# Optimization experiments

Measured on AMD Instinct MI355X. Metric: run time of the kernel, lower is better.

The kernel has to match this reference:

```python
import math
import jax, jax.numpy as jnp
import numpy as np

# TreeAttention (HiP-style hierarchical top-k mask) hyperparameters
K = 64          # self.k: retained keys per query
W0 = 64         # self.w: initial coarse window
SCALE_UP = 2.0
OVERSAMPLE = 1.5
NEG = -32000.0  # masked score fill used inside the pruning loop
FMIN = -1e30    # masked score fill for final softmax


def _gather_rows(m, idx):
    # m: [N, C, H], idx: [N, A, Z] -> [N, A, Z, H]
    return jnp.take_along_axis(m[:, None, :, :], idx[:, :, :, None], axis=2)


def _masked_scores(q, k, xs, xs_mask, value):
    # jax equivalent of masked_bmm_masked_indices (sampled_addmm on a CSR mask):
    # only compute q . k[xs] at the Z listed columns per query row.
    C = k.shape[1]
    kg = _gather_rows(k, jnp.minimum(xs, C - 1))          # [N, A, Z, H]
    s = jnp.einsum('nah,nazh->naz', q, kg)
    return jnp.where(xs_mask > 0.5, s, value)


def _dedup_rows(ps):
    # ps: [R, L] sorted ascending per row. Replicates torch
    # unique_consecutive(return_inverse) + per-row min-subtract + scatter:
    # compact distinct values to the front, fill the rest with -1.
    first = jnp.ones((ps.shape[0], 1), dtype=bool)
    is_new = jnp.concatenate([first, ps[:, 1:] != ps[:, :-1]], axis=1)
    ranks = jnp.cumsum(is_new, axis=1) - 1                # rank of distinct value in row
    rows = jnp.arange(ps.shape[0])[:, None]
    out = jnp.full_like(ps, -1)
    return out.at[rows, ranks].set(ps)  # duplicate ranks write identical values


def _forward_mask(q, k):
    N, T_SRC, HID = k.shape
    _, T_DST, _ = q.shape
    start = T_SRC - T_DST + 1
    tsrcs = jnp.arange(start, start + T_DST, dtype=jnp.float32)[None, :, None]  # [1,T_DST,1]
    w = W0
    ws = jnp.full((N, T_DST, 1), float(W0), dtype=jnp.float32)
    max_pixels = max(int(round(K * OVERSAMPLE)), W0)
    pixels = jnp.broadcast_to(jnp.arange(max_pixels, dtype=jnp.int32)[None, None, :],
                              (N, T_DST, max_pixels))
    pmask = jnp.broadcast_to((jnp.arange(max_pixels) < W0).astype(jnp.float32)[None, None, :],
                             (N, T_DST, max_pixels))
    MAX_SU = int(math.ceil(SCALE_UP))
    while True:  # static loop: w doubles 64 -> 4096, 7 iterations
        is_last = (w == T_SRC)
        Z = pixels.shape[-1]
        # --- topk_mask: score the current candidate pixels, keep top tks ---
        txs = jnp.round(pixels * (tsrcs / ws)).astype(jnp.int32)
        scores = _masked_scores(q, k, txs, pmask, NEG)
        mult = 1.0 if is_last else OVERSAMPLE
        tks = jnp.clip(jnp.round(ws / tsrcs * K * mult), 1.0,
                       jnp.minimum(ws - 1.0, float(Z - 1))).astype(jnp.int32)  # [N,T_DST,1]
        tks_max = int(math.ceil(min(w - 1, Z - 1, K * mult)))
        _, idx = jax.lax.top_k(scores, tks_max)
        new_pixels = jnp.take_along_axis(pixels, idx, axis=-1)
        new_pmask = (jnp.arange(tks_max)[None, None, :] < tks).astype(jnp.float32)
        pixels = jnp.pad(new_pixels, ((0, 0), (0, 0), (0, Z - tks_max)))
        pmask = jnp.pad(new_pmask, ((0, 0), (0, 0), (0, Z - tks_max)))
        # --- update per-row window, then resize pixels into the finer grid ---
        ws_new = jnp.minimum(tsrcs, ws * SCALE_UP)
        scale = ws_new / ws
        ps_start = jnp.round(pixels * scale).astype(jnp.int32)
        ps_end = jnp.round((pixels + 1) * scale).astype(jnp.int32)
        ps = jnp.broadcast_to(ps_start[..., None], (N, T_DST, Z, MAX_SU))
        counts = (ps_end - ps_start)[..., None]
        reps = jnp.arange(MAX_SU, dtype=jnp.float32)[None, None, None, :] * pmask[..., None]
        ps = ps + jnp.minimum(reps, jnp.maximum(counts - 1, 0).astype(jnp.float32)).astype(jnp.int32)
        ps = jnp.sort(ps.reshape(N * T_DST, Z * MAX_SU), axis=-1)
        ps = _dedup_rows(ps).reshape(N, T_DST, -1)
        pmask = (ps >= 0).astype(jnp.float32)
        pixels = jnp.where(ps < 0, 0, ps)
        max_z = K if is_last else int(round(K * 2))
        pixels = pixels[..., :max_z]
        pmask = pmask[..., :max_z]
        ws = ws_new
        if is_last:
            break
        w = min(T_SRC, w * SCALE_UP)
    return pixels, pmask  # CSR mask: per-query column indices + validity mask


def setup_inputs() -> dict:
    key = jax.random.key(0)
    kq, kk, kv = jax.random.split(key, 3)
    N, T_DST, T_SRC, HID = 8, 512, 4096, 64
    q = jax.random.normal(kq, (N, T_DST, HID), dtype=jnp.float32)
    k = jax.random.normal(kk, (N, T_SRC, HID), dtype=jnp.float32)
    v = jax.random.normal(kv, (N, T_SRC, HID), dtype=jnp.float32)
    return {"q": q, "k": k, "v": v}


def reference(q, k, v):
    pixels, pmask = _forward_mask(q, k)          # [N,T_DST,K] int, [N,T_DST,K] {0,1}
    kg = _gather_rows(k, pixels)                 # [N,T_DST,K,H]
    vg = _gather_rows(v, pixels)
    s = jnp.einsum('nah,nazh->naz', q, kg)
    s = jnp.where(pmask > 0.5, s, FMIN)
    p = jax.nn.softmax(s, axis=-1)
    return jnp.einsum('naz,nazh->nah', p, vg)    # [N, T_DST, HID]
```

## Files before the change

kernel.cpp:

```cpp
#include <hip/hip_runtime.h>
#include <math.h>


#define TSRC_N 4096
#define HID_N  64
#define NEGV   -32000.0f

__global__ __launch_bounds__(256)
void tree_attn_kernel(const float* __restrict__ q,
                      const float* __restrict__ k,
                      const float* __restrict__ v,
                      float* __restrict__ out)
{
    const int wid  = __builtin_amdgcn_readfirstlane((int)(threadIdx.x >> 6));
    const int lane = threadIdx.x & 63;
    const int row  = (blockIdx.x << 2) + wid;
    const int n    = row >> 9;
    const float tsrc = (float)(3585 + (row & 511));

    __shared__ __align__(16) unsigned int key_s[4][128];
    __shared__ __align__(16) unsigned int bm[4][128];
    __shared__ int                        pix_s[4][128];
    __shared__ unsigned char              msk_s[4][128];
    __shared__ __align__(8) unsigned int  pp_s[4][128];
    unsigned int* const keyw = key_s[wid];
    unsigned int* const bmw  = bm[wid];
    int* const           pixw = pix_s[wid];
    unsigned char* const mskw = msk_s[wid];
    unsigned int* const  ppw  = pp_s[wid];

    const float* qrow = q + (size_t)row * HID_N;
    const float* kb   = k + (size_t)n * TSRC_N * HID_N;
    const float* vb   = v + (size_t)n * TSRC_N * HID_N;

    auto dot_f32 = [&](int tx) -> float {
        const float4* k4 = (const float4*)(kb + (size_t)tx * HID_N);
        float a0 = 0.f, a1 = 0.f, a2 = 0.f, a3 = 0.f;
        #pragma unroll
        for (int h4 = 0; h4 < HID_N / 4; ++h4) {
            const float4 kv = k4[h4];
            a0 = fmaf(kv.x, qrow[h4 * 4 + 0], a0);
            a1 = fmaf(kv.y, qrow[h4 * 4 + 1], a1);
            a2 = fmaf(kv.z, qrow[h4 * 4 + 2], a2);
            a3 = fmaf(kv.w, qrow[h4 * 4 + 3], a3);
        }
        return (a0 + a1) + (a2 + a3);
    };
    auto flip32 = [](float s) -> unsigned int {
        const unsigned int u = __float_as_uint(s);
        return u ^ ((unsigned)((int)u >> 31) | 0x80000000u);
    };

    pixw[lane]      = lane;
    pixw[lane + 64] = lane + 64;
    mskw[lane]      = 1;
    mskw[lane + 64] = 0;
    __builtin_amdgcn_wave_barrier();

    float ws = 64.0f;
    int Z = 96;

    for (int it = 0; it < 7; ++it) {
        const bool  last    = (it == 6);
        const float mult    = last ? 1.0f : 1.5f;
        const int   tks_max = (it == 0) ? 63 : (last ? 64 : 96);
        const int   max_z   = last ? 64 : 128;
        const int   e1      = lane + 64;

        const float r = tsrc / ws;
        unsigned int key0 = 0, key1 = 0;
        {
            float s0 = NEGV;
            if (mskw[lane]) {
                int tx = (int)rintf((float)pixw[lane] * r);
                tx = tx < (TSRC_N - 1) ? tx : (TSRC_N - 1);
                s0 = dot_f32(tx);
            }
            key0 = flip32(s0);
        }
        if (e1 < Z) {
            float s1 = NEGV;
            if (mskw[e1]) {
                int tx = (int)rintf((float)pixw[e1] * r);
                tx = tx < (TSRC_N - 1) ? tx : (TSRC_N - 1);
                s1 = dot_f32(tx);
            }
            key1 = flip32(s1);
        }
        keyw[lane] = key0;
        keyw[e1]   = key1;
        bmw[lane]  = 0u;
        bmw[e1]    = 0u;
        __builtin_amdgcn_wave_barrier();

        int r0 = 0, r1 = 0;
        #pragma unroll 8
        for (int j = 0; j < 128; j += 4) {
            const uint4 kk = *(const uint4*)&keyw[j];
            r0 += (int)(kk.x > key0) + (int)(kk.y > key0)
                + (int)(kk.z > key0) + (int)(kk.w > key0);
            r1 += (int)(kk.x > key1) + (int)(kk.y > key1)
                + (int)(kk.z > key1) + (int)(kk.w > key1);
        }

        float x = ws / tsrc;
        x *= 64.0f;
        x *= mult;
        float t = rintf(x);
        t = fmaxf(1.0f, fminf(t, fminf(ws - 1.0f, (float)(Z - 1))));
        const int tks = (int)t;

        const float ws_new = fminf(tsrc, ws * 2.0f);
        const float scale  = ws_new / ws;

        if (lane == 0) atomicOr(&bmw[0], 1u);
        if (r0 < tks_max) {
            const int p  = pixw[lane];
            int s0 = (int)rintf((float)p * scale);
            s0 = s0 < (TSRC_N - 1) ? s0 : (TSRC_N - 1);
            atomicOr(&bmw[s0 >> 5], 1u << (s0 & 31));
            if (r0 < tks) {
                const int s1i = (int)rintf((float)(p + 1) * scale);
                if (s1i - s0 >= 2) {
                    const int c = s0 + 1;
                    atomicOr(&bmw[c >> 5], 1u << (c & 31));
                }
            }
        }
        if (e1 < Z && r1 < tks_max) {
            const int p  = pixw[e1];
            int s0 = (int)rintf((float)p * scale);
            s0 = s0 < (TSRC_N - 1) ? s0 : (TSRC_N - 1);
            atomicOr(&bmw[s0 >> 5], 1u << (s0 & 31));
            if (r1 < tks) {
                const int s1i = (int)rintf((float)(p + 1) * scale);
                if (s1i - s0 >= 2) {
                    const int c = s0 + 1;
                    atomicOr(&bmw[c >> 5], 1u << (c & 31));
                }
            }
        }
        __builtin_amdgcn_wave_barrier();

        const uint2 w2 = *(const uint2*)&bmw[2 * lane];
        const int c = __popc(w2.x) + __popc(w2.y);
        int scan = c;
        #pragma unroll
        for (int off = 1; off < 64; off <<= 1) {
            const int o = __shfl_up(scan, off);
            if (lane >= off) scan += o;
        }
        int pref = scan - c;
        pixw[lane] = 0;  pixw[e1] = 0;
        mskw[lane] = 0;  mskw[e1] = 0;
        __builtin_amdgcn_wave_barrier();

        unsigned int wv = w2.x;
        int base = lane << 6;
        while (wv) {
            if (pref >= max_z) break;
            const int b = __ffs(wv) - 1;
            wv &= wv - 1u;
            pixw[pref] = base + b;
            mskw[pref] = 1;
            ++pref;
        }
        wv = w2.y;
        base += 32;
        while (wv) {
            if (pref >= max_z) break;
            const int b = __ffs(wv) - 1;
            wv &= wv - 1u;
            pixw[pref] = base + b;
            mskw[pref] = 1;
            ++pref;
        }
        __builtin_amdgcn_wave_barrier();

        ws = ws_new;
        Z  = max_z;
    }

    {
        const int pix = pixw[lane];
        float sfin = -1e30f;
        if (mskw[lane]) sfin = dot_f32(pix);
        float m = sfin;
        #pragma unroll
        for (int off = 32; off > 0; off >>= 1)
            m = fmaxf(m, __shfl_xor(m, off));
        const float e = __expf(sfin - m);
        float ssum = e;
        #pragma unroll
        for (int off = 32; off > 0; off >>= 1)
            ssum += __shfl_xor(ssum, off);
        const float p = e / ssum;
        ppw[2 * lane]     = __float_as_uint(p);
        ppw[2 * lane + 1] = (unsigned int)pix;
    }
    __builtin_amdgcn_wave_barrier();

    {
        float acc = 0.f;
        #pragma unroll 4
        for (int j = 0; j < 64; ++j) {
            const uint2 pp = *(const uint2*)&ppw[2 * j];
            acc = fmaf(__uint_as_float(pp.x),
                       vb[(size_t)pp.y * HID_N + lane], acc);
        }
        out[(size_t)row * HID_N + lane] = acc;
    }
}

extern "C" void kernel_launch(void* const* d_in, const int* in_sizes, int n_in,
                              void* d_out, int out_size, void* d_ws, size_t ws_size,
                              hipStream_t stream) {
    const float* q = (const float*)d_in[0];
    const float* k = (const float*)d_in[1];
    const float* v = (const float*)d_in[2];
    float* out = (float*)d_out;
    const int rows = in_sizes[0] / HID_N;
    tree_attn_kernel<<<(rows + 3) / 4, 256, 0, stream>>>(q, k, v, out);
}
```

Baseline: 163.9 us.

## Split each query row across two wavefronts with block-level sync

Each query row is now handled by a pair of wavefronts instead of one, so each lane scores one candidate instead of two. The final PV accumulation is split across the pair and combined through shared memory. The dot product is software-pipelined with explicit prefetch, and launch bounds now request higher occupancy. The cost is wave-level barriers replaced by block-wide __syncthreads, twice as many blocks, and the redundant prefix scan and compaction now run in both waves of a pair.

```diff
diff --git a/kernel.cpp b/kernel.cpp
--- a/kernel.cpp
+++ b/kernel.cpp
@@ -6,28 +6,34 @@
 #define HID_N  64
 #define NEGV   -32000.0f
 
-__global__ __launch_bounds__(256)
+__global__ __launch_bounds__(256, 8)
 void tree_attn_kernel(const float* __restrict__ q,
                       const float* __restrict__ k,
                       const float* __restrict__ v,
                       float* __restrict__ out)
 {
-    const int wid  = __builtin_amdgcn_readfirstlane((int)(threadIdx.x >> 6));
+    const int wid4 = __builtin_amdgcn_readfirstlane((int)(threadIdx.x >> 6));
     const int lane = threadIdx.x & 63;
-    const int row  = (blockIdx.x << 2) + wid;
+    const int pairid = wid4 >> 1;
+    const int sub    = wid4 & 1;
+    const int row  = (blockIdx.x << 1) + pairid;
     const int n    = row >> 9;
     const float tsrc = (float)(3585 + (row & 511));
-
-    __shared__ __align__(16) unsigned int key_s[4][128];
-    __shared__ __align__(16) unsigned int bm[4][128];
-    __shared__ int                        pix_s[4][128];
-    __shared__ unsigned char              msk_s[4][128];
-    __shared__ __align__(8) unsigned int  pp_s[4][128];
-    unsigned int* const keyw = key_s[wid];
-    unsigned int* const bmw  = bm[wid];
-    int* const           pixw = pix_s[wid];
-    unsigned char* const mskw = msk_s[wid];
-    unsigned int* const  ppw  = pp_s[wid];
+    const int e    = (sub << 6) + lane;
+
+    __shared__ __align__(16) unsigned int key_s[2][128];
+    __shared__ __align__(16) unsigned int bm_s[2][128];
+    __shared__ int                        pix_s[2][128];
+    __shared__ unsigned char              msk_s[2][128];
+    __shared__ __align__(8) unsigned int  pp_s[2][128];
+    __shared__ float                      part_s[2][64];
+
+    unsigned int*  const keyw  = key_s[pairid];
+    unsigned int*  const bmw   = bm_s[pairid];
+    int*           const pixw  = pix_s[pairid];
+    unsigned char* const mskw  = msk_s[pairid];
+    unsigned int*  const ppw   = pp_s[pairid];
+    float*         const partw = part_s[pairid];
 
     const float* qrow = q + (size_t)row * HID_N;
     const float* kb   = k + (size_t)n * TSRC_N * HID_N;
@@ -35,14 +41,24 @@
 
     auto dot_f32 = [&](int tx) -> float {
         const float4* k4 = (const float4*)(kb + (size_t)tx * HID_N);
+        float4 c0 = k4[0], c1 = k4[1], c2 = k4[2], c3 = k4[3];
         float a0 = 0.f, a1 = 0.f, a2 = 0.f, a3 = 0.f;
         #pragma unroll
-        for (int h4 = 0; h4 < HID_N / 4; ++h4) {
-            const float4 kv = k4[h4];
-            a0 = fmaf(kv.x, qrow[h4 * 4 + 0], a0);
-            a1 = fmaf(kv.y, qrow[h4 * 4 + 1], a1);
-            a2 = fmaf(kv.z, qrow[h4 * 4 + 2], a2);
-            a3 = fmaf(kv.w, qrow[h4 * 4 + 3], a3);
+        for (int g = 0; g < 4; ++g) {
+            float4 n0, n1, n2, n3;
+            if (g < 3) {
+                n0 = k4[4*g+4]; n1 = k4[4*g+5]; n2 = k4[4*g+6]; n3 = k4[4*g+7];
+            }
+            const float* qg = qrow + 16*g;
+            a0 = fmaf(c0.x, qg[0],  a0);  a1 = fmaf(c0.y, qg[1],  a1);
+            a2 = fmaf(c0.z, qg[2],  a2);  a3 = fmaf(c0.w, qg[3],  a3);
+            a0 = fmaf(c1.x, qg[4],  a0);  a1 = fmaf(c1.y, qg[5],  a1);
+            a2 = fmaf(c1.z, qg[6],  a2);  a3 = fmaf(c1.w, qg[7],  a3);
+            a0 = fmaf(c2.x, qg[8],  a0);  a1 = fmaf(c2.y, qg[9],  a1);
+            a2 = fmaf(c2.z, qg[10], a2);  a3 = fmaf(c2.w, qg[11], a3);
+            a0 = fmaf(c3.x, qg[12], a0);  a1 = fmaf(c3.y, qg[13], a1);
+            a2 = fmaf(c3.z, qg[14], a2);  a3 = fmaf(c3.w, qg[15], a3);
+            if (g < 3) { c0 = n0; c1 = n1; c2 = n2; c3 = n3; }
         }
         return (a0 + a1) + (a2 + a3);
     };
@@ -51,11 +67,9 @@
         return u ^ ((unsigned)((int)u >> 31) | 0x80000000u);
     };
 
-    pixw[lane]      = lane;
-    pixw[lane + 64] = lane + 64;
-    mskw[lane]      = 1;
-    mskw[lane + 64] = 0;
-    __builtin_amdgcn_wave_barrier();
+    pixw[e] = e;
+    mskw[e] = (e < 64) ? 1 : 0;
+    __syncthreads();
 
     float ws = 64.0f;
     int Z = 96;
@@ -65,42 +79,39 @@
         const float mult    = last ? 1.0f : 1.5f;
         const int   tks_max = (it == 0) ? 63 : (last ? 64 : 96);
         const int   max_z   = last ? 64 : 128;
-        const int   e1      = lane + 64;
 
         const float r = tsrc / ws;
-        unsigned int key0 = 0, key1 = 0;
-        {
-            float s0 = NEGV;
-            if (mskw[lane]) {
-                int tx = (int)rintf((float)pixw[lane] * r);
+        unsigned int mykey = 0;
+        int myp = 0;
+        if (e < Z) {
+            float sc = NEGV;
+            myp = pixw[e];
+            if (mskw[e]) {
+                int tx = (int)rintf((float)myp * r);
                 tx = tx < (TSRC_N - 1) ? tx : (TSRC_N - 1);
-                s0 = dot_f32(tx);
+                sc = dot_f32(tx);
             }
-            key0 = flip32(s0);
-        }
-        if (e1 < Z) {
-            float s1 = NEGV;
-            if (mskw[e1]) {
-                int tx = (int)rintf((float)pixw[e1] * r);
-                tx = tx < (TSRC_N - 1) ? tx : (TSRC_N - 1);
-                s1 = dot_f32(tx);
-            }
-            key1 = flip32(s1);
-        }
-        keyw[lane] = key0;
-        keyw[e1]   = key1;
-        bmw[lane]  = 0u;
-        bmw[e1]    = 0u;
-        __builtin_amdgcn_wave_barrier();
-
-        int r0 = 0, r1 = 0;
-        #pragma unroll 8
-        for (int j = 0; j < 128; j += 4) {
-            const uint4 kk = *(const uint4*)&keyw[j];
-            r0 += (int)(kk.x > key0) + (int)(kk.y > key0)
-                + (int)(kk.z > key0) + (int)(kk.w > key0);
-            r1 += (int)(kk.x > key1) + (int)(kk.y > key1)
-                + (int)(kk.z > key1) + (int)(kk.w > key1);
+            mykey = flip32(sc);
+        }
+        keyw[e] = mykey;
+        bmw[e]  = 0u;
+        __syncthreads();
+
+        int rank = 0;
+        #pragma unroll
+        for (int j = 0; j < 128; j += 16) {
+            const uint4 a = *(const uint4*)&keyw[j];
+            const uint4 b = *(const uint4*)&keyw[j + 4];
+            const uint4 c = *(const uint4*)&keyw[j + 8];
+            const uint4 d = *(const uint4*)&keyw[j + 12];
+            rank += (int)(a.x > mykey) + (int)(a.y > mykey)
+                  + (int)(a.z > mykey) + (int)(a.w > mykey)
+                  + (int)(b.x > mykey) + (int)(b.y > mykey)
+                  + (int)(b.z > mykey) + (int)(b.w > mykey)
+                  + (int)(c.x > mykey) + (int)(c.y > mykey)
+                  + (int)(c.z > mykey) + (int)(c.w > mykey)
+                  + (int)(d.x > mykey) + (int)(d.y > mykey)
+                  + (int)(d.z > mykey) + (int)(d.w > mykey);
         }
 
         float x = ws / tsrc;
@@ -113,47 +124,33 @@
         const float ws_new = fminf(tsrc, ws * 2.0f);
         const float scale  = ws_new / ws;
 
-        if (lane == 0) atomicOr(&bmw[0], 1u);
-        if (r0 < tks_max) {
-            const int p  = pixw[lane];
-            int s0 = (int)rintf((float)p * scale);
+        if (e == 0) atomicOr(&bmw[0], 1u);
+        if (e < Z && rank < tks_max) {
+            int s0 = (int)rintf((float)myp * scale);
             s0 = s0 < (TSRC_N - 1) ? s0 : (TSRC_N - 1);
             atomicOr(&bmw[s0 >> 5], 1u << (s0 & 31));
-            if (r0 < tks) {
-                const int s1i = (int)rintf((float)(p + 1) * scale);
+            if (rank < tks) {
+                const int s1i = (int)rintf((float)(myp + 1) * scale);
                 if (s1i - s0 >= 2) {
-                    const int c = s0 + 1;
-                    atomicOr(&bmw[c >> 5], 1u << (c & 31));
+                    const int c2 = s0 + 1;
+                    atomicOr(&bmw[c2 >> 5], 1u << (c2 & 31));
                 }
             }
         }
-        if (e1 < Z && r1 < tks_max) {
-            const int p  = pixw[e1];
-            int s0 = (int)rintf((float)p * scale);
-            s0 = s0 < (TSRC_N - 1) ? s0 : (TSRC_N - 1);
-            atomicOr(&bmw[s0 >> 5], 1u << (s0 & 31));
-            if (r1 < tks) {
-                const int s1i = (int)rintf((float)(p + 1) * scale);
-                if (s1i - s0 >= 2) {
-                    const int c = s0 + 1;
-                    atomicOr(&bmw[c >> 5], 1u << (c & 31));
-                }
-            }
-        }
-        __builtin_amdgcn_wave_barrier();
+        __syncthreads();
 
         const uint2 w2 = *(const uint2*)&bmw[2 * lane];
-        const int c = __popc(w2.x) + __popc(w2.y);
-        int scan = c;
+        const int cnt = __popc(w2.x) + __popc(w2.y);
+        int scan = cnt;
         #pragma unroll
         for (int off = 1; off < 64; off <<= 1) {
             const int o = __shfl_up(scan, off);
             if (lane >= off) scan += o;
         }
-        int pref = scan - c;
-        pixw[lane] = 0;  pixw[e1] = 0;
-        mskw[lane] = 0;  mskw[e1] = 0;
-        __builtin_amdgcn_wave_barrier();
+        int pref = scan - cnt;
+        pixw[e] = 0;
+        mskw[e] = 0;
+        __syncthreads();
 
         unsigned int wv = w2.x;
         int base = lane << 6;
@@ -181,35 +178,47 @@
         Z  = max_z;
     }
 
-    {
-        const int pix = pixw[lane];
+    if (sub == 0) {
+        const int pixf = pixw[lane];
         float sfin = -1e30f;
-        if (mskw[lane]) sfin = dot_f32(pix);
+        if (mskw[lane]) sfin = dot_f32(pixf);
         float m = sfin;
         #pragma unroll
         for (int off = 32; off > 0; off >>= 1)
             m = fmaxf(m, __shfl_xor(m, off));
-        const float e = __expf(sfin - m);
-        float ssum = e;
+        const float ex = __expf(sfin - m);
+        float ssum = ex;
         #pragma unroll
         for (int off = 32; off > 0; off >>= 1)
             ssum += __shfl_xor(ssum, off);
-        const float p = e / ssum;
+        const float p = ex / ssum;
         ppw[2 * lane]     = __float_as_uint(p);
-        ppw[2 * lane + 1] = (unsigned int)pix;
+        ppw[2 * lane + 1] = (unsigned int)pixf;
     }
-    __builtin_amdgcn_wave_barrier();
-
+    __syncthreads();
+
+    float acc = 0.f;
     {
-        float acc = 0.f;
-        #pragma unroll 4
-        for (int j = 0; j < 64; ++j) {
-            const uint2 pp = *(const uint2*)&ppw[2 * j];
-            acc = fmaf(__uint_as_float(pp.x),
-                       vb[(size_t)pp.y * HID_N + lane], acc);
-        }
-        out[(size_t)row * HID_N + lane] = acc;
+        const unsigned int* pbase = ppw + (sub << 6);
+        #pragma unroll
+        for (int j0 = 0; j0 < 32; j0 += 4) {
+            const uint2 p0 = *(const uint2*)&pbase[2 * j0];
+            const uint2 p1 = *(const uint2*)&pbase[2 * j0 + 2];
+            const uint2 p2 = *(const uint2*)&pbase[2 * j0 + 4];
+            const uint2 p3 = *(const uint2*)&pbase[2 * j0 + 6];
+            const float v0 = vb[(size_t)p0.y * HID_N + lane];
+            const float v1 = vb[(size_t)p1.y * HID_N + lane];
+            const float v2 = vb[(size_t)p2.y * HID_N + lane];
+            const float v3 = vb[(size_t)p3.y * HID_N + lane];
+            acc = fmaf(__uint_as_float(p0.x), v0, acc);
+            acc = fmaf(__uint_as_float(p1.x), v1, acc);
+            acc = fmaf(__uint_as_float(p2.x), v2, acc);
+            acc = fmaf(__uint_as_float(p3.x), v3, acc);
+        }
     }
+    if (sub == 1) partw[lane] = acc;
+    __syncthreads();
+    if (sub == 0) out[(size_t)row * HID_N + lane] = acc + partw[lane];
 }
 
 extern "C" void kernel_launch(void* const* d_in, const int* in_sizes, int n_in,
@@ -220,5 +229,5 @@
     const float* v = (const float*)d_in[2];
     float* out = (float*)d_out;
     const int rows = in_sizes[0] / HID_N;
-    tree_attn_kernel<<<(rows + 3) / 4, 256, 0, stream>>>(q, k, v, out);
+    tree_attn_kernel<<<(rows + 1) / 2, 256, 0, stream>>>(q, k, v, out);
 }
```

Result: slower. 515.8 us (+214.8%).

## Compute key dot products cooperatively with 8 lanes per key row

Applied to the files above, without the earlier changes.

Replaces the per-lane full 64-element dot product, where each lane streamed a whole 256-byte key row with scalar q loads, with an 8-lane cooperative dot. Each lane reads two float4 of the key row, holds its q slice in registers, and reduces with xor shuffles. Scores go through shared memory before ranking. The aim is coalesced key row reads and no repeated q loads. The V accumulation loop is also unrolled to issue four gathers before using them, at the cost of more loop iterations and shuffle overhead per candidate.

```diff
diff --git a/kernel.cpp b/kernel.cpp
--- a/kernel.cpp
+++ b/kernel.cpp
@@ -17,34 +17,42 @@
     const int row  = (blockIdx.x << 2) + wid;
     const int n    = row >> 9;
     const float tsrc = (float)(3585 + (row & 511));
+    const int sg = lane >> 3;
+    const int sl = lane & 7;
 
     __shared__ __align__(16) unsigned int key_s[4][128];
-    __shared__ __align__(16) unsigned int bm[4][128];
+    __shared__ __align__(16) unsigned int bm_s[4][128];
     __shared__ int                        pix_s[4][128];
     __shared__ unsigned char              msk_s[4][128];
     __shared__ __align__(8) unsigned int  pp_s[4][128];
-    unsigned int* const keyw = key_s[wid];
-    unsigned int* const bmw  = bm[wid];
-    int* const           pixw = pix_s[wid];
+    unsigned int*  const keyw = key_s[wid];
+    unsigned int*  const bmw  = bm_s[wid];
+    int*           const pixw = pix_s[wid];
     unsigned char* const mskw = msk_s[wid];
-    unsigned int* const  ppw  = pp_s[wid];
+    unsigned int*  const ppw  = pp_s[wid];
 
     const float* qrow = q + (size_t)row * HID_N;
     const float* kb   = k + (size_t)n * TSRC_N * HID_N;
     const float* vb   = v + (size_t)n * TSRC_N * HID_N;
 
-    auto dot_f32 = [&](int tx) -> float {
-        const float4* k4 = (const float4*)(kb + (size_t)tx * HID_N);
-        float a0 = 0.f, a1 = 0.f, a2 = 0.f, a3 = 0.f;
-        #pragma unroll
-        for (int h4 = 0; h4 < HID_N / 4; ++h4) {
-            const float4 kv = k4[h4];
-            a0 = fmaf(kv.x, qrow[h4 * 4 + 0], a0);
-            a1 = fmaf(kv.y, qrow[h4 * 4 + 1], a1);
-            a2 = fmaf(kv.z, qrow[h4 * 4 + 2], a2);
-            a3 = fmaf(kv.w, qrow[h4 * 4 + 3], a3);
-        }
-        return (a0 + a1) + (a2 + a3);
+    const float4 q0 = ((const float4*)qrow)[2 * sl];
+    const float4 q1 = ((const float4*)qrow)[2 * sl + 1];
+
+    auto coop_dot = [&](int tx) -> float {
+        const float4* kp = (const float4*)(kb + (size_t)tx * HID_N) + 2 * sl;
+        const float4 k0 = kp[0];
+        const float4 k1 = kp[1];
+        float a0 = fmaf(k0.x, q0.x, k0.y * q0.y);
+        float a1 = fmaf(k0.z, q0.z, k0.w * q0.w);
+        a0 = fmaf(k1.x, q1.x, a0);
+        a1 = fmaf(k1.y, q1.y, a1);
+        a0 = fmaf(k1.z, q1.z, a0);
+        a1 = fmaf(k1.w, q1.w, a1);
+        float s = a0 + a1;
+        s += __shfl_xor(s, 1);
+        s += __shfl_xor(s, 2);
+        s += __shfl_xor(s, 4);
+        return s;
     };
     auto flip32 = [](float s) -> unsigned int {
         const unsigned int u = __float_as_uint(s);
@@ -65,42 +73,52 @@
         const float mult    = last ? 1.0f : 1.5f;
         const int   tks_max = (it == 0) ? 63 : (last ? 64 : 96);
         const int   max_z   = last ? 64 : 128;
-        const int   e1      = lane + 64;
 
         const float r = tsrc / ws;
-        unsigned int key0 = 0, key1 = 0;
-        {
-            float s0 = NEGV;
-            if (mskw[lane]) {
-                int tx = (int)rintf((float)pixw[lane] * r);
-                tx = tx < (TSRC_N - 1) ? tx : (TSRC_N - 1);
-                s0 = dot_f32(tx);
+        #pragma unroll 4
+        for (int p = 0; p < 16; ++p) {
+            const int c = (p << 3) + sg;
+            unsigned int key = 0;
+            if (c < Z) {
+                float sc = NEGV;
+                if (mskw[c]) {
+                    int tx = (int)rintf((float)pixw[c] * r);
+                    tx = tx < (TSRC_N - 1) ? tx : (TSRC_N - 1);
+                    sc = coop_dot(tx);
+                }
+                key = flip32(sc);
             }
-            key0 = flip32(s0);
-        }
-        if (e1 < Z) {
-            float s1 = NEGV;
-            if (mskw[e1]) {
-                int tx = (int)rintf((float)pixw[e1] * r);
-                tx = tx < (TSRC_N - 1) ? tx : (TSRC_N - 1);
-                s1 = dot_f32(tx);
-            }
-            key1 = flip32(s1);
-        }
-        keyw[lane] = key0;
-        keyw[e1]   = key1;
-        bmw[lane]  = 0u;
-        bmw[e1]    = 0u;
-        __builtin_amdgcn_wave_barrier();
-
+            if (sl == 0) keyw[c] = key;
+        }
+        bmw[lane]      = 0u;
+        bmw[lane + 64] = 0u;
+        __builtin_amdgcn_wave_barrier();
+
+        const unsigned int key0 = keyw[lane];
+        const unsigned int key1 = keyw[lane + 64];
         int r0 = 0, r1 = 0;
-        #pragma unroll 8
-        for (int j = 0; j < 128; j += 4) {
-            const uint4 kk = *(const uint4*)&keyw[j];
-            r0 += (int)(kk.x > key0) + (int)(kk.y > key0)
-                + (int)(kk.z > key0) + (int)(kk.w > key0);
-            r1 += (int)(kk.x > key1) + (int)(kk.y > key1)
-                + (int)(kk.z > key1) + (int)(kk.w > key1);
+        #pragma unroll
+        for (int j = 0; j < 128; j += 16) {
+            const uint4 a = *(const uint4*)&keyw[j];
+            const uint4 b = *(const uint4*)&keyw[j + 4];
+            const uint4 c = *(const uint4*)&keyw[j + 8];
+            const uint4 d = *(const uint4*)&keyw[j + 12];
+            r0 += (int)(a.x > key0) + (int)(a.y > key0)
+                + (int)(a.z > key0) + (int)(a.w > key0)
+                + (int)(b.x > key0) + (int)(b.y > key0)
+                + (int)(b.z > key0) + (int)(b.w > key0)
+                + (int)(c.x > key0) + (int)(c.y > key0)
+                + (int)(c.z > key0) + (int)(c.w > key0)
+                + (int)(d.x > key0) + (int)(d.y > key0)
+                + (int)(d.z > key0) + (int)(d.w > key0);
+            r1 += (int)(a.x > key1) + (int)(a.y > key1)
+                + (int)(a.z > key1) + (int)(a.w > key1)
+                + (int)(b.x > key1) + (int)(b.y > key1)
+                + (int)(b.z > key1) + (int)(b.w > key1)
+                + (int)(c.x > key1) + (int)(c.y > key1)
+                + (int)(c.z > key1) + (int)(c.w > key1)
+                + (int)(d.x > key1) + (int)(d.y > key1)
+                + (int)(d.z > key1) + (int)(d.w > key1);
         }
 
         float x = ws / tsrc;
@@ -115,44 +133,44 @@
 
         if (lane == 0) atomicOr(&bmw[0], 1u);
         if (r0 < tks_max) {
-            const int p  = pixw[lane];
-            int s0 = (int)rintf((float)p * scale);
+            const int p0 = pixw[lane];
+            int s0 = (int)rintf((float)p0 * scale);
             s0 = s0 < (TSRC_N - 1) ? s0 : (TSRC_N - 1);
             atomicOr(&bmw[s0 >> 5], 1u << (s0 & 31));
             if (r0 < tks) {
-                const int s1i = (int)rintf((float)(p + 1) * scale);
+                const int s1i = (int)rintf((float)(p0 + 1) * scale);
                 if (s1i - s0 >= 2) {
-                    const int c = s0 + 1;
-                    atomicOr(&bmw[c >> 5], 1u << (c & 31));
+                    const int c2 = s0 + 1;
+                    atomicOr(&bmw[c2 >> 5], 1u << (c2 & 31));
                 }
             }
         }
-        if (e1 < Z && r1 < tks_max) {
-            const int p  = pixw[e1];
-            int s0 = (int)rintf((float)p * scale);
+        if (lane + 64 < Z && r1 < tks_max) {
+            const int p1 = pixw[lane + 64];
+            int s0 = (int)rintf((float)p1 * scale);
             s0 = s0 < (TSRC_N - 1) ? s0 : (TSRC_N - 1);
             atomicOr(&bmw[s0 >> 5], 1u << (s0 & 31));
             if (r1 < tks) {
-                const int s1i = (int)rintf((float)(p + 1) * scale);
+                const int s1i = (int)rintf((float)(p1 + 1) * scale);
                 if (s1i - s0 >= 2) {
-                    const int c = s0 + 1;
-                    atomicOr(&bmw[c >> 5], 1u << (c & 31));
+                    const int c2 = s0 + 1;
+                    atomicOr(&bmw[c2 >> 5], 1u << (c2 & 31));
                 }
             }
         }
         __builtin_amdgcn_wave_barrier();
 
         const uint2 w2 = *(const uint2*)&bmw[2 * lane];
-        const int c = __popc(w2.x) + __popc(w2.y);
-        int scan = c;
+        const int cnt = __popc(w2.x) + __popc(w2.y);
+        int scan = cnt;
         #pragma unroll
         for (int off = 1; off < 64; off <<= 1) {
             const int o = __shfl_up(scan, off);
             if (lane >= off) scan += o;
         }
-        int pref = scan - c;
-        pixw[lane] = 0;  pixw[e1] = 0;
-        mskw[lane] = 0;  mskw[e1] = 0;
+        int pref = scan - cnt;
+        pixw[lane] = 0;  pixw[lane + 64] = 0;
+        mskw[lane] = 0;  mskw[lane + 64] = 0;
         __builtin_amdgcn_wave_barrier();
 
         unsigned int wv = w2.x;
@@ -181,32 +199,48 @@
         Z  = max_z;
     }
 
+    #pragma unroll 4
+    for (int p = 0; p < 8; ++p) {
+        const int c = (p << 3) + sg;
+        float sc = -1e30f;
+        if (mskw[c]) sc = coop_dot(pixw[c]);
+        if (sl == 0) keyw[c] = __float_as_uint(sc);
+    }
+    __builtin_amdgcn_wave_barrier();
+
     {
-        const int pix = pixw[lane];
-        float sfin = -1e30f;
-        if (mskw[lane]) sfin = dot_f32(pix);
+        const float sfin = __uint_as_float(keyw[lane]);
         float m = sfin;
         #pragma unroll
         for (int off = 32; off > 0; off >>= 1)
             m = fmaxf(m, __shfl_xor(m, off));
-        const float e = __expf(sfin - m);
-        float ssum = e;
+        const float ex = __expf(sfin - m);
+        float ssum = ex;
         #pragma unroll
         for (int off = 32; off > 0; off >>= 1)
             ssum += __shfl_xor(ssum, off);
-        const float p = e / ssum;
-        ppw[2 * lane]     = __float_as_uint(p);
-        ppw[2 * lane + 1] = (unsigned int)pix;
+        const float pr = ex / ssum;
+        ppw[2 * lane]     = __float_as_uint(pr);
+        ppw[2 * lane + 1] = (unsigned int)pixw[lane];
     }
     __builtin_amdgcn_wave_barrier();
 
     {
         float acc = 0.f;
         #pragma unroll 4
-        for (int j = 0; j < 64; ++j) {
-            const uint2 pp = *(const uint2*)&ppw[2 * j];
-            acc = fmaf(__uint_as_float(pp.x),
-                       vb[(size_t)pp.y * HID_N + lane], acc);
+        for (int j0 = 0; j0 < 64; j0 += 4) {
+            const uint2 p0 = *(const uint2*)&ppw[2 * j0];
+            const uint2 p1 = *(const uint2*)&ppw[2 * j0 + 2];
+            const uint2 p2 = *(const uint2*)&ppw[2 * j0 + 4];
+            const uint2 p3 = *(const uint2*)&ppw[2 * j0 + 6];
+            const float v0 = vb[(size_t)p0.y * HID_N + lane];
+            const float v1 = vb[(size_t)p1.y * HID_N + lane];
+            const float v2 = vb[(size_t)p2.y * HID_N + lane];
+            const float v3 = vb[(size_t)p3.y * HID_N + lane];
+            acc = fmaf(__uint_as_float(p0.x), v0, acc);
+            acc = fmaf(__uint_as_float(p1.x), v1, acc);
+            acc = fmaf(__uint_as_float(p2.x), v2, acc);
+            acc = fmaf(__uint_as_float(p3.x), v3, acc);
         }
         out[(size_t)row * HID_N + lane] = acc;
     }
```

After: 207.5 us. 26.6% more time.
